# Performance work log

Hardware: AMD Instinct MI355X
Metric: run time of the kernel (lower is better)

## Reference

```python
import jax, jax.numpy as jnp
import numpy as np
import math

DIMS = 128
VOXEL_SIZE = 4.0
QUANT_SIZE = 0.02
QUANT_LEN = int((2 * VOXEL_SIZE + 0.0001) // QUANT_SIZE)  # 400
N = 1024


def setup_inputs() -> dict:
    key = jax.random.key(0)
    k1, k2, k3, k4, k5, k6 = jax.random.split(key, 6)
    features = jax.random.normal(k1, (N, DIMS), dtype=jnp.float32)
    # distances uniform in [-voxel_size, voxel_size)
    voxel_distances = (jax.random.uniform(k2, (N, N, 3), dtype=jnp.float32) * 2.0 - 1.0) * VOXEL_SIZE
    W_qkv = jax.random.normal(k3, (DIMS, 3 * DIMS), dtype=jnp.float32) * 0.02
    b_qkv = jnp.zeros((3 * DIMS,), dtype=jnp.float32)
    table_x = jax.random.normal(k4, (3, QUANT_LEN, DIMS), dtype=jnp.float32) * 0.02
    table_y = jax.random.normal(k5, (3, QUANT_LEN, DIMS), dtype=jnp.float32) * 0.02
    table_z = jax.random.normal(k6, (3, QUANT_LEN, DIMS), dtype=jnp.float32) * 0.02
    return {"features": features, "voxel_distances": voxel_distances,
            "W_qkv": W_qkv, "b_qkv": b_qkv,
            "table_x": table_x, "table_y": table_y, "table_z": table_z}


def reference(features, voxel_distances, W_qkv, b_qkv, table_x, table_y, table_z):
    n, dims = features.shape
    qkv = (features @ W_qkv + b_qkv).reshape(n, 3, dims)
    q, k, v = qkv[:, 0], qkv[:, 1], qkv[:, 2]  # each [N, D]

    # quantized distance indices, clamped like torch's .clamp(max=...)
    max_idx = VOXEL_SIZE * 2.0 / QUANT_SIZE - 1.0  # 399
    idx = jnp.floor((voxel_distances + VOXEL_SIZE) / QUANT_SIZE)
    idx = jnp.clip(idx, 0.0, max_idx).astype(jnp.int32)  # [N, N, 3]

    # gathered positional encoding: [N, N, D]
    encode_k = table_x[1][idx[:, :, 0]] + table_y[1][idx[:, :, 1]] + table_z[1][idx[:, :, 2]]
    # bias[i, j] = k[i] . encode_k[i, j]  (faithful to k[:, None] @ encode_k^T)
    position_bias = jnp.einsum('id,ijd->ij', k, encode_k)

    scores = (q @ k.T + position_bias) / math.sqrt(dims)
    attn = jax.nn.softmax(scores, axis=-1)  # [N, N]
    return attn @ v  # [N, D]
```

## Files before the change

kernel.cpp:

```cpp
#include <hip/hip_runtime.h>
#include <math.h>

#define N_PTS 1024
#define D 128
#define QL 400
#define PLD 1200
#define SQRT_D_INV 0.08838834764831845f

typedef __attribute__((ext_vector_type(8))) short bf16x8;
typedef __attribute__((ext_vector_type(4))) float f32x4;
typedef unsigned short u16;

#define GLOBAL_AS __attribute__((address_space(1)))
#define LDS_AS    __attribute__((address_space(3)))

__device__ __forceinline__ u16 f2bf(float x) {
    union { float f; unsigned u; } v; v.f = x;
    unsigned r = v.u + 0x7fff + ((v.u >> 16) & 1);
    return (u16)(r >> 16);
}
__device__ __forceinline__ float b2f(u16 h) {
    union { unsigned u; float f; } v; v.u = ((unsigned)h) << 16;
    return v.f;
}

__global__ __launch_bounds__(256) void prep_kernel(
    const float* __restrict__ features, const float* __restrict__ W,
    const float* __restrict__ bias,
    const float* __restrict__ tx, const float* __restrict__ ty,
    const float* __restrict__ tz,
    u16* __restrict__ qb, u16* __restrict__ kb, u16* __restrict__ vT,
    u16* __restrict__ Tcat)
{
    __shared__ __align__(16) u16 As[64 * 128];
    __shared__ __align__(16) u16 Bs[64 * 128];
    const int tid = threadIdx.x;
    const int bx = blockIdx.x;

    if (bx >= 96) {
        int e0 = (bx - 96) * 1024 + tid * 4;
        int n = e0 >> 7, k = e0 & 127;
        int sec = n / QL, r = n - sec * QL;
        const float* t = (sec == 0) ? tx : ((sec == 1) ? ty : tz);
        float4 v = *(const float4*)&t[QL * D + r * D + k];
        ushort4 o;
        o.x = f2bf(v.x); o.y = f2bf(v.y); o.z = f2bf(v.z); o.w = f2bf(v.w);
        *(ushort4*)&Tcat[e0] = o;
        return;
    }

    const int wave = tid >> 6, lane = tid & 63;
    const int wr = wave >> 1, wc = wave & 1;
    const int l15 = lane & 15, l4 = lane >> 4;
    const int bm = (bx / 6) * 64;
    const int bn = (bx % 6) * 64;

    #pragma unroll
    for (int r0 = 0; r0 < 4; ++r0) {
        int unit = r0 * 256 + tid;
        int row = unit >> 4, c16 = unit & 15;
        const float* ga = features + (size_t)(bm + row) * D + c16 * 8;
        float4 a0 = *(const float4*)ga;
        float4 a1 = *(const float4*)(ga + 4);
        u16 h[8] = {f2bf(a0.x), f2bf(a0.y), f2bf(a0.z), f2bf(a0.w),
                    f2bf(a1.x), f2bf(a1.y), f2bf(a1.z), f2bf(a1.w)};
        *(bf16x8*)(As + row * 128 + ((c16 ^ (row & 7)) * 8)) = *(bf16x8*)h;
    }
    #pragma unroll
    for (int r2 = 0; r2 < 8; ++r2) {
        int k = r2 * 16 + (tid >> 4);
        int nl = (tid & 15) * 4;
        float4 w4 = *(const float4*)&W[(size_t)k * 384 + bn + nl];
        float wv[4] = {w4.x, w4.y, w4.z, w4.w};
        #pragma unroll
        for (int e = 0; e < 4; ++e) {
            int n = nl + e;
            Bs[n * 128 + (((k >> 3) ^ (n & 7)) << 3) + (k & 7)] = f2bf(wv[e]);
        }
    }
    __syncthreads();

    f32x4 acc[2][2] = {};
    #pragma unroll
    for (int ks = 0; ks < 4; ++ks) {
        bf16x8 a[2], b[2];
        #pragma unroll
        for (int m = 0; m < 2; ++m) {
            int row = wr * 32 + m * 16 + l15;
            int c16 = ks * 4 + l4;
            a[m] = *(const bf16x8*)(As + row * 128 + ((c16 ^ (row & 7)) * 8));
        }
        #pragma unroll
        for (int n = 0; n < 2; ++n) {
            int row = wc * 32 + n * 16 + l15;
            int c16 = ks * 4 + l4;
            b[n] = *(const bf16x8*)(Bs + row * 128 + ((c16 ^ (row & 7)) * 8));
        }
        #pragma unroll
        for (int m = 0; m < 2; ++m)
            #pragma unroll
            for (int n = 0; n < 2; ++n)
                acc[m][n] = __builtin_amdgcn_mfma_f32_16x16x32_bf16(
                    a[m], b[n], acc[m][n], 0, 0, 0);
    }

    #pragma unroll
    for (int m = 0; m < 2; ++m)
        #pragma unroll
        for (int n = 0; n < 2; ++n)
            #pragma unroll
            for (int r = 0; r < 4; ++r) {
                int grow = bm + wr * 32 + m * 16 + l4 * 4 + r;
                int gcol = bn + wc * 32 + n * 16 + l15;
                float val = acc[m][n][r] + bias[gcol];
                int reg = gcol >> 7, lc = gcol & 127;
                if (reg == 0)      qb[grow * D + lc] = f2bf(val * SQRT_D_INV);
                else if (reg == 1) kb[grow * D + lc] = f2bf(val);
                else               vT[(size_t)lc * N_PTS + grow] = f2bf(val);
            }
}

__global__ __launch_bounds__(256) void p_gemm_kernel(
    const u16* __restrict__ A,
    const u16* __restrict__ B,
    u16* __restrict__ Cb,
    unsigned* __restrict__ cnt)
{
    __shared__ __align__(16) u16 As[64 * 128];
    __shared__ __align__(16) u16 Bs[64 * 128];
    const int tid  = threadIdx.x;
    if (blockIdx.x == 0 && blockIdx.y == 0 && tid < 64) cnt[tid] = 0u;
    const int wave = tid >> 6, lane = tid & 63;
    const int wr = wave >> 1, wc = wave & 1;
    const int l15 = lane & 15, l4 = lane >> 4;
    const int bm = blockIdx.y * 64, bn = blockIdx.x * 64;

    #pragma unroll
    for (int r = 0; r < 4; ++r) {
        int unit = r * 256 + tid;
        int row  = unit >> 4;
        int c16  = unit & 15;
        int csw  = c16 ^ (row & 7);
        const u16* ga = A + (size_t)(bm + row) * D + csw * 8;
        __builtin_amdgcn_global_load_lds(
            (const GLOBAL_AS unsigned int*)ga,
            (LDS_AS unsigned int*)(As + r * 2048 + wave * 512), 16, 0, 0);
        int brow = bn + row; if (brow > PLD - 1) brow = PLD - 1;
        const u16* gb = B + (size_t)brow * D + csw * 8;
        __builtin_amdgcn_global_load_lds(
            (const GLOBAL_AS unsigned int*)gb,
            (LDS_AS unsigned int*)(Bs + r * 2048 + wave * 512), 16, 0, 0);
    }
    __syncthreads();

    f32x4 acc[2][2] = {};
    #pragma unroll
    for (int ks = 0; ks < 4; ++ks) {
        bf16x8 a[2], b[2];
        #pragma unroll
        for (int m = 0; m < 2; ++m) {
            int row = wr * 32 + m * 16 + l15;
            int c16 = ks * 4 + l4;
            a[m] = *(const bf16x8*)(As + row * 128 + ((c16 ^ (row & 7)) * 8));
        }
        #pragma unroll
        for (int n = 0; n < 2; ++n) {
            int row = wc * 32 + n * 16 + l15;
            int c16 = ks * 4 + l4;
            b[n] = *(const bf16x8*)(Bs + row * 128 + ((c16 ^ (row & 7)) * 8));
        }
        #pragma unroll
        for (int m = 0; m < 2; ++m)
            #pragma unroll
            for (int n = 0; n < 2; ++n)
                acc[m][n] = __builtin_amdgcn_mfma_f32_16x16x32_bf16(
                    a[m], b[n], acc[m][n], 0, 0, 0);
    }

    #pragma unroll
    for (int m = 0; m < 2; ++m)
        #pragma unroll
        for (int n = 0; n < 2; ++n)
            #pragma unroll
            for (int r = 0; r < 4; ++r) {
                int grow = bm + wr * 32 + m * 16 + l4 * 4 + r;
                int gcol = bn + wc * 32 + n * 16 + l15;
                if (gcol < PLD)
                    Cb[(size_t)grow * PLD + gcol] = f2bf(acc[m][n][r] * SQRT_D_INV);
            }
}

__global__ __launch_bounds__(256) void flash_kernel(
    const u16* __restrict__ qb,
    const u16* __restrict__ kb,
    const u16* __restrict__ vT,
    const u16* __restrict__ Pb,
    const float* __restrict__ vd,
    float* __restrict__ part,
    float* __restrict__ rowsumC,
    unsigned* __restrict__ cnt,
    float* __restrict__ out)
{
    __shared__ __align__(16) u16 Pl[2432 * 8];
    __shared__ __align__(16) u16 Ps[16 * 128];
    __shared__ float rsw[4][16];
    __shared__ int lastflag;
    const int tid = threadIdx.x;
    const int wave = tid >> 6, lane = tid & 63;
    const int l15 = lane & 15, l4 = lane >> 4;
    const int it = blockIdx.x;
    const int chunk = blockIdx.y;
    const int bm = it * 16;
    const int bn = chunk * 128;

    const u16* Pg = Pb + (size_t)bm * PLD;
    #pragma unroll
    for (int r0 = 0; r0 < 9; ++r0) {
        int unit = r0 * 256 + tid;
        __builtin_amdgcn_global_load_lds(
            (const GLOBAL_AS unsigned int*)(Pg + unit * 8),
            (LDS_AS unsigned int*)(Pl + r0 * 2048 + wave * 512), 16, 0, 0);
    }
    if (wave < 2) {
        int unit = 9 * 256 + tid;
        int cu = unit > 2399 ? 2399 : unit;
        __builtin_amdgcn_global_load_lds(
            (const GLOBAL_AS unsigned int*)(Pg + cu * 8),
            (LDS_AS unsigned int*)(Pl + 9 * 2048 + wave * 512), 16, 0, 0);
    }

    float vx[2][4], vy[2][4], vz[2][4];
    #pragma unroll
    for (int nn = 0; nn < 2; ++nn)
        #pragma unroll
        for (int r = 0; r < 4; ++r) {
            int i = l4 * 4 + r;
            int j = wave * 32 + nn * 16 + l15;
            const float* vp = vd + ((size_t)(bm + i) * N_PTS + bn + j) * 3;
            vx[nn][r] = vp[0]; vy[nn][r] = vp[1]; vz[nn][r] = vp[2];
        }

    bf16x8 aq[4];
    #pragma unroll
    for (int ks = 0; ks < 4; ++ks)
        aq[ks] = *(const bf16x8*)(qb + (size_t)(bm + l15) * D + ks * 32 + l4 * 8);
    f32x4 acc[2] = {};
    #pragma unroll
    for (int nn = 0; nn < 2; ++nn) {
        int jt = bn + wave * 32 + nn * 16;
        #pragma unroll
        for (int ks = 0; ks < 4; ++ks) {
            bf16x8 bk = *(const bf16x8*)(kb + (size_t)(jt + l15) * D + ks * 32 + l4 * 8);
            acc[nn] = __builtin_amdgcn_mfma_f32_16x16x32_bf16(aq[ks], bk, acc[nn], 0, 0, 0);
        }
    }
    __syncthreads();

    float rs[4] = {0.f, 0.f, 0.f, 0.f};
    #pragma unroll
    for (int nn = 0; nn < 2; ++nn)
        #pragma unroll
        for (int r = 0; r < 4; ++r) {
            int i = l4 * 4 + r;
            int jl = wave * 32 + nn * 16 + l15;
            int ix = (int)floorf((vx[nn][r] + 4.0f) * 50.0f);
            int iy = (int)floorf((vy[nn][r] + 4.0f) * 50.0f);
            int iz = (int)floorf((vz[nn][r] + 4.0f) * 50.0f);
            ix = min(max(ix, 0), QL - 1);
            iy = min(max(iy, 0), QL - 1);
            iz = min(max(iz, 0), QL - 1);
            const u16* Pr = Pl + i * PLD;
            float bv = b2f(Pr[ix]) + b2f(Pr[QL + iy]) + b2f(Pr[2 * QL + iz]);
            float e = __expf(acc[nn][r] + bv);
            rs[r] += e;
            Ps[i * 128 + (((jl >> 3) ^ (i & 7)) * 8) + (jl & 7)] = f2bf(e);
        }
    #pragma unroll
    for (int r = 0; r < 4; ++r)
        #pragma unroll
        for (int off = 1; off < 16; off <<= 1)
            rs[r] += __shfl_xor(rs[r], off);
    if (l15 == 0)
        #pragma unroll
        for (int r = 0; r < 4; ++r) rsw[wave][l4 * 4 + r] = rs[r];
    __syncthreads();
    if (tid < 16)
        rowsumC[(it * 8 + chunk) * 16 + tid] =
            rsw[0][tid] + rsw[1][tid] + rsw[2][tid] + rsw[3][tid];

    bf16x8 pa[4];
    #pragma unroll
    for (int kt = 0; kt < 4; ++kt)
        pa[kt] = *(const bf16x8*)(Ps + l15 * 128 + (((kt * 4 + l4) ^ (l15 & 7)) * 8));
    f32x4 acc2[2] = {};
    #pragma unroll
    for (int nn = 0; nn < 2; ++nn) {
        int dt = wave * 32 + nn * 16;
        #pragma unroll
        for (int kt = 0; kt < 4; ++kt) {
            bf16x8 bv8 = *(const bf16x8*)(vT + (size_t)(dt + l15) * N_PTS + bn + kt * 32 + l4 * 8);
            acc2[nn] = __builtin_amdgcn_mfma_f32_16x16x32_bf16(pa[kt], bv8, acc2[nn], 0, 0, 0);
        }
    }
    float* po = part + (size_t)(it * 8 + chunk) * (16 * D);
    #pragma unroll
    for (int nn = 0; nn < 2; ++nn)
        #pragma unroll
        for (int r = 0; r < 4; ++r)
            po[(l4 * 4 + r) * D + wave * 32 + nn * 16 + l15] = acc2[nn][r];

    asm volatile("s_waitcnt vmcnt(0)" ::: "memory");
    __syncthreads();
    if (tid == 0) {
        unsigned old = __hip_atomic_fetch_add(
            &cnt[it], 1u, __ATOMIC_RELAXED, __HIP_MEMORY_SCOPE_AGENT);
        lastflag = (old == 7u);
    }
    __syncthreads();
    if (lastflag) {
        const float4* p4 = (const float4*)(part + (size_t)it * 8 * 16 * D);
        const float* rsb = rowsumC + it * 8 * 16;
        #pragma unroll
        for (int h = 0; h < 2; ++h) {
            int f4 = h * 256 + tid;
            int row = f4 >> 5;
            float rsum = 0.0f;
            #pragma unroll
            for (int z = 0; z < 8; ++z) rsum += rsb[z * 16 + row];
            float inv = 1.0f / rsum;
            float4 a = p4[f4];
            #pragma unroll
            for (int z = 1; z < 8; ++z) {
                float4 v = p4[z * 512 + f4];
                a.x += v.x; a.y += v.y; a.z += v.z; a.w += v.w;
            }
            a.x *= inv; a.y *= inv; a.z *= inv; a.w *= inv;
            ((float4*)out)[bm * 32 + f4] = a;
        }
    }
}

extern "C" void kernel_launch(void* const* d_in, const int* in_sizes, int n_in,
                              void* d_out, int out_size, void* d_ws, size_t ws_size,
                              hipStream_t stream)
{
    const float* features = (const float*)d_in[0];
    const float* vd       = (const float*)d_in[1];
    const float* W        = (const float*)d_in[2];
    const float* b        = (const float*)d_in[3];
    const float* tx       = (const float*)d_in[4];
    const float* ty       = (const float*)d_in[5];
    const float* tz       = (const float*)d_in[6];
    float* out = (float*)d_out;

    char* w0 = (char*)d_ws;
    unsigned* cnt = (unsigned*)w0;
    u16* qb       = (u16*)(w0 + 0x1000);
    u16* kb       = (u16*)(w0 + 0x50000);
    u16* vT       = (u16*)(w0 + 0x90000);
    u16* Tcat     = (u16*)(w0 + 0xD0000);
    u16* Pb       = (u16*)(w0 + 0x120000);
    float* part   = (float*)(w0 + 0x380000);
    float* rowsumC= (float*)(w0 + 0x780000);

    dim3 blk(256);

    prep_kernel<<<dim3(246), blk, 0, stream>>>(
        features, W, b, tx, ty, tz, qb, kb, vT, Tcat);

    p_gemm_kernel<<<dim3(19, 16), blk, 0, stream>>>(kb, Tcat, Pb, cnt);

    flash_kernel<<<dim3(64, 8), blk, 0, stream>>>(
        qb, kb, vT, Pb, vd, part, rowsumC, cnt, out);
}
```

Measured before the change: 25.48 us.

## Fuse QKV projection and position-table GEMM into one prep kernel

```diff
diff --git a/kernel.cpp b/kernel.cpp
--- a/kernel.cpp
+++ b/kernel.cpp
@@ -24,37 +24,178 @@
     return v.f;
 }
 
-__global__ __launch_bounds__(256) void prep_kernel(
+__global__ __launch_bounds__(256) void prep2_kernel(
     const float* __restrict__ features, const float* __restrict__ W,
     const float* __restrict__ bias,
     const float* __restrict__ tx, const float* __restrict__ ty,
     const float* __restrict__ tz,
     u16* __restrict__ qb, u16* __restrict__ kb, u16* __restrict__ vT,
-    u16* __restrict__ Tcat)
+    u16* __restrict__ Pb, unsigned* __restrict__ cnt)
 {
-    __shared__ __align__(16) u16 As[64 * 128];
-    __shared__ __align__(16) u16 Bs[64 * 128];
+    __shared__ __align__(16) u16 smem[24704];
     const int tid = threadIdx.x;
     const int bx = blockIdx.x;
-
-    if (bx >= 96) {
-        int e0 = (bx - 96) * 1024 + tid * 4;
-        int n = e0 >> 7, k = e0 & 127;
-        int sec = n / QL, r = n - sec * QL;
-        const float* t = (sec == 0) ? tx : ((sec == 1) ? ty : tz);
-        float4 v = *(const float4*)&t[QL * D + r * D + k];
-        ushort4 o;
-        o.x = f2bf(v.x); o.y = f2bf(v.y); o.z = f2bf(v.z); o.w = f2bf(v.w);
-        *(ushort4*)&Tcat[e0] = o;
-        return;
-    }
-
     const int wave = tid >> 6, lane = tid & 63;
     const int wr = wave >> 1, wc = wave & 1;
     const int l15 = lane & 15, l4 = lane >> 4;
-    const int bm = (bx / 6) * 64;
-    const int bn = (bx % 6) * 64;
-
+
+    if (bx == 0 && tid < 64) cnt[tid] = 0u;
+
+    if (bx < 96) {
+        u16* As = smem;
+        u16* Bs = smem + 8192;
+        const int bm = (bx / 6) * 64;
+        const int bn = (bx % 6) * 64;
+
+        #pragma unroll
+        for (int r0 = 0; r0 < 4; ++r0) {
+            int unit = r0 * 256 + tid;
+            int row = unit >> 4, c16 = unit & 15;
+            const float* ga = features + (size_t)(bm + row) * D + c16 * 8;
+            float4 a0 = *(const float4*)ga;
+            float4 a1 = *(const float4*)(ga + 4);
+            u16 h[8] = {f2bf(a0.x), f2bf(a0.y), f2bf(a0.z), f2bf(a0.w),
+                        f2bf(a1.x), f2bf(a1.y), f2bf(a1.z), f2bf(a1.w)};
+            *(bf16x8*)(As + row * 128 + ((c16 ^ (row & 7)) * 8)) = *(bf16x8*)h;
+        }
+        #pragma unroll
+        for (int r2 = 0; r2 < 8; ++r2) {
+            int k = r2 * 16 + (tid >> 4);
+            int nl = (tid & 15) * 4;
+            float4 w4 = *(const float4*)&W[(size_t)k * 384 + bn + nl];
+            float wv[4] = {w4.x, w4.y, w4.z, w4.w};
+            #pragma unroll
+            for (int e = 0; e < 4; ++e) {
+                int n = nl + e;
+                Bs[n * 128 + (((k >> 3) ^ (n & 7)) << 3) + (k & 7)] = f2bf(wv[e]);
+            }
+        }
+        __syncthreads();
+
+        f32x4 acc[2][2] = {};
+        #pragma unroll
+        for (int ks = 0; ks < 4; ++ks) {
+            bf16x8 a[2], b[2];
+            #pragma unroll
+            for (int m = 0; m < 2; ++m) {
+                int row = wr * 32 + m * 16 + l15;
+                int c16 = ks * 4 + l4;
+                a[m] = *(const bf16x8*)(As + row * 128 + ((c16 ^ (row & 7)) * 8));
+            }
+            #pragma unroll
+            for (int n = 0; n < 2; ++n) {
+                int row = wc * 32 + n * 16 + l15;
+                int c16 = ks * 4 + l4;
+                b[n] = *(const bf16x8*)(Bs + row * 128 + ((c16 ^ (row & 7)) * 8));
+            }
+            #pragma unroll
+            for (int m = 0; m < 2; ++m)
+                #pragma unroll
+                for (int n = 0; n < 2; ++n)
+                    acc[m][n] = __builtin_amdgcn_mfma_f32_16x16x32_bf16(
+                        a[m], b[n], acc[m][n], 0, 0, 0);
+        }
+
+        #pragma unroll
+        for (int m = 0; m < 2; ++m)
+            #pragma unroll
+            for (int n = 0; n < 2; ++n)
+                #pragma unroll
+                for (int r = 0; r < 4; ++r) {
+                    int grow = bm + wr * 32 + m * 16 + l4 * 4 + r;
+                    int gcol = bn + wc * 32 + n * 16 + l15;
+                    float val = acc[m][n][r] + bias[gcol];
+                    int reg = gcol >> 7, lc = gcol & 127;
+                    if (reg == 0)      qb[grow * D + lc] = f2bf(val * SQRT_D_INV);
+                    else if (reg == 1) kb[grow * D + lc] = f2bf(val);
+                    else               vT[(size_t)lc * N_PTS + grow] = f2bf(val);
+                }
+        return;
+    }
+
+    const int t = bx - 96;
+    const int ib = t / 19, jb = t % 19;
+    const int bm = ib * 64, bn = jb * 64;
+    u16* Ta = smem;
+    u16* Wb = smem + 8192;
+    float* bPl = (float*)(smem + 24576);
+
+    #pragma unroll
+    for (int r0 = 0; r0 < 4; ++r0) {
+        int unit = r0 * 256 + tid;
+        int row = unit >> 4, c16 = unit & 15;
+        int c = bn + row; if (c > PLD - 1) c = PLD - 1;
+        int sec = c / QL, rr = c - sec * QL;
+        const float* tsec = (sec == 0) ? tx : ((sec == 1) ? ty : tz);
+        const float* ga = tsec + QL * D + rr * D + c16 * 8;
+        float4 a0 = *(const float4*)ga;
+        float4 a1 = *(const float4*)(ga + 4);
+        u16 h[8] = {f2bf(a0.x), f2bf(a0.y), f2bf(a0.z), f2bf(a0.w),
+                    f2bf(a1.x), f2bf(a1.y), f2bf(a1.z), f2bf(a1.w)};
+        *(bf16x8*)(Ta + row * 128 + ((c16 ^ (row & 7)) * 8)) = *(bf16x8*)h;
+    }
+    #pragma unroll
+    for (int r0 = 0; r0 < 8; ++r0) {
+        int unit = r0 * 256 + tid;
+        int e = unit >> 4, c16 = unit & 15;
+        const float* ga = W + (size_t)e * 384 + 128 + c16 * 8;
+        float4 a0 = *(const float4*)ga;
+        float4 a1 = *(const float4*)(ga + 4);
+        u16 h[8] = {f2bf(a0.x), f2bf(a0.y), f2bf(a0.z), f2bf(a0.w),
+                    f2bf(a1.x), f2bf(a1.y), f2bf(a1.z), f2bf(a1.w)};
+        *(bf16x8*)(Wb + e * 128 + ((c16 ^ (e & 7)) * 8)) = *(bf16x8*)h;
+    }
+    __syncthreads();
+
+    f32x4 accG[2][4] = {};
+    #pragma unroll
+    for (int ks = 0; ks < 4; ++ks) {
+        bf16x8 a[2], bfr[4];
+        #pragma unroll
+        for (int m = 0; m < 2; ++m) {
+            int row = wr * 32 + m * 16 + l15;
+            int c16 = ks * 4 + l4;
+            a[m] = *(const bf16x8*)(Ta + row * 128 + ((c16 ^ (row & 7)) * 8));
+        }
+        #pragma unroll
+        for (int n = 0; n < 4; ++n) {
+            int e = wc * 64 + n * 16 + l15;
+            int c16 = ks * 4 + l4;
+            bfr[n] = *(const bf16x8*)(Wb + e * 128 + ((c16 ^ (e & 7)) * 8));
+        }
+        #pragma unroll
+        for (int m = 0; m < 2; ++m)
+            #pragma unroll
+            for (int n = 0; n < 4; ++n)
+                accG[m][n] = __builtin_amdgcn_mfma_f32_16x16x32_bf16(
+                    a[m], bfr[n], accG[m][n], 0, 0, 0);
+    }
+
+    float bsum = 0.0f;
+    {
+        int c_l = tid >> 2, q = tid & 3;
+        #pragma unroll
+        for (int dd = 0; dd < 32; ++dd) {
+            int d = q * 32 + dd;
+            u16 tv = Ta[c_l * 128 + (((d >> 3) ^ (c_l & 7)) * 8) + (d & 7)];
+            bsum += b2f(tv) * bias[128 + d];
+        }
+        bsum += __shfl_xor(bsum, 1);
+        bsum += __shfl_xor(bsum, 2);
+    }
+    __syncthreads();
+
+    #pragma unroll
+    for (int m = 0; m < 2; ++m)
+        #pragma unroll
+        for (int n = 0; n < 4; ++n)
+            #pragma unroll
+            for (int rr = 0; rr < 4; ++rr) {
+                int c_l = wr * 32 + m * 16 + l4 * 4 + rr;
+                int e   = wc * 64 + n * 16 + l15;
+                Wb[c_l * 128 + (((e >> 3) ^ (c_l & 7)) * 8) + (e & 7)] =
+                    f2bf(accG[m][n][rr]);
+            }
     #pragma unroll
     for (int r0 = 0; r0 < 4; ++r0) {
         int unit = r0 * 256 + tid;
@@ -64,129 +205,46 @@
         float4 a1 = *(const float4*)(ga + 4);
         u16 h[8] = {f2bf(a0.x), f2bf(a0.y), f2bf(a0.z), f2bf(a0.w),
                     f2bf(a1.x), f2bf(a1.y), f2bf(a1.z), f2bf(a1.w)};
-        *(bf16x8*)(As + row * 128 + ((c16 ^ (row & 7)) * 8)) = *(bf16x8*)h;
-    }
-    #pragma unroll
-    for (int r2 = 0; r2 < 8; ++r2) {
-        int k = r2 * 16 + (tid >> 4);
-        int nl = (tid & 15) * 4;
-        float4 w4 = *(const float4*)&W[(size_t)k * 384 + bn + nl];
-        float wv[4] = {w4.x, w4.y, w4.z, w4.w};
-        #pragma unroll
-        for (int e = 0; e < 4; ++e) {
-            int n = nl + e;
-            Bs[n * 128 + (((k >> 3) ^ (n & 7)) << 3) + (k & 7)] = f2bf(wv[e]);
-        }
-    }
+        *(bf16x8*)(Ta + row * 128 + ((c16 ^ (row & 7)) * 8)) = *(bf16x8*)h;
+    }
+    if ((tid & 3) == 0) bPl[tid >> 2] = bsum;
     __syncthreads();
 
     f32x4 acc[2][2] = {};
     #pragma unroll
     for (int ks = 0; ks < 4; ++ks) {
-        bf16x8 a[2], b[2];
+        bf16x8 a[2], bq[2];
         #pragma unroll
         for (int m = 0; m < 2; ++m) {
             int row = wr * 32 + m * 16 + l15;
             int c16 = ks * 4 + l4;
-            a[m] = *(const bf16x8*)(As + row * 128 + ((c16 ^ (row & 7)) * 8));
+            a[m] = *(const bf16x8*)(Ta + row * 128 + ((c16 ^ (row & 7)) * 8));
         }
         #pragma unroll
         for (int n = 0; n < 2; ++n) {
-            int row = wc * 32 + n * 16 + l15;
+            int crow = wc * 32 + n * 16 + l15;
             int c16 = ks * 4 + l4;
-            b[n] = *(const bf16x8*)(Bs + row * 128 + ((c16 ^ (row & 7)) * 8));
+            bq[n] = *(const bf16x8*)(Wb + crow * 128 + ((c16 ^ (crow & 7)) * 8));
         }
         #pragma unroll
         for (int m = 0; m < 2; ++m)
             #pragma unroll
             for (int n = 0; n < 2; ++n)
                 acc[m][n] = __builtin_amdgcn_mfma_f32_16x16x32_bf16(
-                    a[m], b[n], acc[m][n], 0, 0, 0);
-    }
-
+                    a[m], bq[n], acc[m][n], 0, 0, 0);
+    }
     #pragma unroll
     for (int m = 0; m < 2; ++m)
         #pragma unroll
         for (int n = 0; n < 2; ++n)
             #pragma unroll
-            for (int r = 0; r < 4; ++r) {
-                int grow = bm + wr * 32 + m * 16 + l4 * 4 + r;
+            for (int rr = 0; rr < 4; ++rr) {
+                int grow = bm + wr * 32 + m * 16 + l4 * 4 + rr;
                 int gcol = bn + wc * 32 + n * 16 + l15;
-                float val = acc[m][n][r] + bias[gcol];
-                int reg = gcol >> 7, lc = gcol & 127;
-                if (reg == 0)      qb[grow * D + lc] = f2bf(val * SQRT_D_INV);
-                else if (reg == 1) kb[grow * D + lc] = f2bf(val);
-                else               vT[(size_t)lc * N_PTS + grow] = f2bf(val);
-            }
-}
-
-__global__ __launch_bounds__(256) void p_gemm_kernel(
-    const u16* __restrict__ A,
-    const u16* __restrict__ B,
-    u16* __restrict__ Cb,
-    unsigned* __restrict__ cnt)
-{
-    __shared__ __align__(16) u16 As[64 * 128];
-    __shared__ __align__(16) u16 Bs[64 * 128];
-    const int tid  = threadIdx.x;
-    if (blockIdx.x == 0 && blockIdx.y == 0 && tid < 64) cnt[tid] = 0u;
-    const int wave = tid >> 6, lane = tid & 63;
-    const int wr = wave >> 1, wc = wave & 1;
-    const int l15 = lane & 15, l4 = lane >> 4;
-    const int bm = blockIdx.y * 64, bn = blockIdx.x * 64;
-
-    #pragma unroll
-    for (int r = 0; r < 4; ++r) {
-        int unit = r * 256 + tid;
-        int row  = unit >> 4;
-        int c16  = unit & 15;
-        int csw  = c16 ^ (row & 7);
-        const u16* ga = A + (size_t)(bm + row) * D + csw * 8;
-        __builtin_amdgcn_global_load_lds(
-            (const GLOBAL_AS unsigned int*)ga,
-            (LDS_AS unsigned int*)(As + r * 2048 + wave * 512), 16, 0, 0);
-        int brow = bn + row; if (brow > PLD - 1) brow = PLD - 1;
-        const u16* gb = B + (size_t)brow * D + csw * 8;
-        __builtin_amdgcn_global_load_lds(
-            (const GLOBAL_AS unsigned int*)gb,
-            (LDS_AS unsigned int*)(Bs + r * 2048 + wave * 512), 16, 0, 0);
-    }
-    __syncthreads();
-
-    f32x4 acc[2][2] = {};
-    #pragma unroll
-    for (int ks = 0; ks < 4; ++ks) {
-        bf16x8 a[2], b[2];
-        #pragma unroll
-        for (int m = 0; m < 2; ++m) {
-            int row = wr * 32 + m * 16 + l15;
-            int c16 = ks * 4 + l4;
-            a[m] = *(const bf16x8*)(As + row * 128 + ((c16 ^ (row & 7)) * 8));
-        }
-        #pragma unroll
-        for (int n = 0; n < 2; ++n) {
-            int row = wc * 32 + n * 16 + l15;
-            int c16 = ks * 4 + l4;
-            b[n] = *(const bf16x8*)(Bs + row * 128 + ((c16 ^ (row & 7)) * 8));
-        }
-        #pragma unroll
-        for (int m = 0; m < 2; ++m)
-            #pragma unroll
-            for (int n = 0; n < 2; ++n)
-                acc[m][n] = __builtin_amdgcn_mfma_f32_16x16x32_bf16(
-                    a[m], b[n], acc[m][n], 0, 0, 0);
-    }
-
-    #pragma unroll
-    for (int m = 0; m < 2; ++m)
-        #pragma unroll
-        for (int n = 0; n < 2; ++n)
-            #pragma unroll
-            for (int r = 0; r < 4; ++r) {
-                int grow = bm + wr * 32 + m * 16 + l4 * 4 + r;
-                int gcol = bn + wc * 32 + n * 16 + l15;
+                int c_l  = wc * 32 + n * 16 + l15;
                 if (gcol < PLD)
-                    Cb[(size_t)grow * PLD + gcol] = f2bf(acc[m][n][r] * SQRT_D_INV);
+                    Pb[(size_t)grow * PLD + gcol] =
+                        f2bf((acc[m][n][rr] + bPl[c_l]) * SQRT_D_INV);
             }
 }
 
@@ -358,17 +416,14 @@
     u16* qb       = (u16*)(w0 + 0x1000);
     u16* kb       = (u16*)(w0 + 0x50000);
     u16* vT       = (u16*)(w0 + 0x90000);
-    u16* Tcat     = (u16*)(w0 + 0xD0000);
-    u16* Pb       = (u16*)(w0 + 0x120000);
-    float* part   = (float*)(w0 + 0x380000);
-    float* rowsumC= (float*)(w0 + 0x780000);
+    u16* Pb       = (u16*)(w0 + 0xD0000);
+    float* part   = (float*)(w0 + 0x330000);
+    float* rowsumC= (float*)(w0 + 0x730000);
 
     dim3 blk(256);
 
-    prep_kernel<<<dim3(246), blk, 0, stream>>>(
-        features, W, b, tx, ty, tz, qb, kb, vT, Tcat);
-
-    p_gemm_kernel<<<dim3(19, 16), blk, 0, stream>>>(kb, Tcat, Pb, cnt);
+    prep2_kernel<<<dim3(400), blk, 0, stream>>>(
+        features, W, b, tx, ty, tz, qb, kb, vT, Pb, cnt);
 
     flash_kernel<<<dim3(64, 8), blk, 0, stream>>>(
         qb, kb, vT, Pb, vd, part, rowsumC, cnt, out);
```

After: 23.85 us. 6.4% less time.
